# Kernel tuning notes

Measured on AMD Instinct MI355X. Metric: run time of the kernel, lower is better.

Reference implementation:

```python
import jax, jax.numpy as jnp
import numpy as np

N_NODES = 100000
N_EDGES = 3200000


def gcn_conv(x, src, dst, W, b, n):
    # x: [N, Fin] -> linear transform then symmetric-normalized scatter-add (PyG GCNConv)
    xw = x @ W  # [N, Fout]
    loop = jnp.arange(n, dtype=src.dtype)
    s = jnp.concatenate([src, loop])  # add self-loops
    d = jnp.concatenate([dst, loop])
    deg = jax.ops.segment_sum(jnp.ones_like(s, dtype=xw.dtype), d, num_segments=n)
    dinv = jnp.where(deg > 0, jax.lax.rsqrt(deg), 0.0)
    norm = dinv[s] * dinv[d]  # [E+N]
    out = jax.ops.segment_sum(xw[s] * norm[:, None], d, num_segments=n)
    return out + b


def setup_inputs() -> dict:
    key = jax.random.key(0)
    ks = jax.random.split(key, 11)
    x = jax.random.normal(ks[0], (N_NODES, 2), dtype=jnp.float32)
    edge_index = jax.random.randint(ks[1], (2, N_EDGES), 0, N_NODES, dtype=jnp.int64)
    W1 = jax.random.normal(ks[2], (2, 32), dtype=jnp.float32) * 0.5
    b1 = jax.random.normal(ks[3], (32,), dtype=jnp.float32) * 0.1
    W2 = jax.random.normal(ks[4], (32, 32), dtype=jnp.float32) * 0.18
    b2 = jax.random.normal(ks[5], (32,), dtype=jnp.float32) * 0.1
    Wf1 = jax.random.normal(ks[6], (32, 32), dtype=jnp.float32) * 0.18
    bf1 = jax.random.normal(ks[7], (32,), dtype=jnp.float32) * 0.1
    Wf2 = jax.random.normal(ks[8], (32, 1), dtype=jnp.float32) * 0.18
    bf2 = jax.random.normal(ks[9], (1,), dtype=jnp.float32) * 0.1
    return {"x": x, "edge_index": edge_index, "W1": W1, "b1": b1, "W2": W2,
            "b2": b2, "Wf1": Wf1, "bf1": bf1, "Wf2": Wf2, "bf2": bf2}


def reference(x, edge_index, W1, b1, W2, b2, Wf1, bf1, Wf2, bf2):
    n = x.shape[0]
    src, dst = edge_index[0], edge_index[1]
    h = jax.nn.relu(gcn_conv(x, src, dst, W1, b1, n))
    h = jax.nn.relu(gcn_conv(h, src, dst, W2, b2, n))
    h = jax.nn.relu(h @ Wf1 + bf1)
    return h @ Wf2 + bf2  # [N, 1]
```

## Files before the change

kernel.cpp:

```cpp
#include <hip/hip_runtime.h>

#define NGRP 512
#define CAP  6656
#define EPB  8192
#define SRC_BITS 17
#define SRC_MASK 0x1FFFF

static __device__ __forceinline__ unsigned short f2bf(float f) {
    unsigned u = __float_as_uint(f);
    return (unsigned short)((u + 0x7FFFu + ((u >> 16) & 1u)) >> 16);
}
static __device__ __forceinline__ float bf2f_lo(unsigned u) { return __uint_as_float(u << 16); }
static __device__ __forceinline__ float bf2f_hi(unsigned u) { return __uint_as_float(u & 0xFFFF0000u); }


__global__ void k_init(int* gcursor) {
    int t = threadIdx.x;
    gcursor[t] = t * CAP;
}

__global__ __launch_bounds__(512) void k_partition(const int* __restrict__ ei, int* gcursor,
                                                   unsigned* __restrict__ pairs,
                                                   int E, int n, int GN) {
    __shared__ int cnt[NGRP];
    __shared__ int cur[NGRP];
    int tid = threadIdx.x;
    cnt[tid] = 0;
    __syncthreads();
    int base = blockIdx.x * EPB;
    for (int k = tid; k < EPB; k += 512) {
        int e = base + k;
        if (e < E) {
            int s = ei[e], d = ei[E + e];
            if ((unsigned)s < (unsigned)n && (unsigned)d < (unsigned)n)
                atomicAdd(&cnt[d / GN], 1);
        }
    }
    __syncthreads();
    { int c = cnt[tid]; cur[tid] = c ? atomicAdd(&gcursor[tid], c) : 0; }
    __syncthreads();
    for (int k = tid; k < EPB; k += 512) {
        int e = base + k;
        if (e < E) {
            int s = ei[e], d = ei[E + e];
            if ((unsigned)s < (unsigned)n && (unsigned)d < (unsigned)n) {
                int g = d / GN;
                int w = atomicAdd(&cur[g], 1);
                if (w < (g + 1) * CAP)
                    pairs[w] = ((unsigned)(d - g * GN) << SRC_BITS) | (unsigned)s;
            }
        }
    }
}

__global__ __launch_bounds__(512) void k_build(const int* __restrict__ gcursor,
                                               const unsigned* __restrict__ pairs,
                                               const float2* __restrict__ x2,
                                               int* __restrict__ rowStart, int* __restrict__ rowEnd,
                                               int* __restrict__ srclist, float* __restrict__ dinv,
                                               float2* __restrict__ z, int n, int GN) {
    __shared__ unsigned pl[CAP];
    __shared__ int cnt[512];
    __shared__ int cur[512];
    int g = blockIdx.x;
    int t = threadIdx.x;
    int gbeg = g * CAP;
    int gend = gcursor[g];
    int cape = gbeg + CAP;
    if (gend > cape) gend = cape;
    int m = gend - gbeg;
    cnt[t] = 0;
    __syncthreads();
    for (int k = t; k < m; k += 512) {
        unsigned v = pairs[gbeg + k];
        pl[k] = v;
        atomicAdd(&cnt[(v >> SRC_BITS) & 511], 1);
    }
    __syncthreads();
    int c = cnt[t];
    for (int off = 1; off < 512; off <<= 1) {
        int add = (t >= off) ? cnt[t - off] : 0;
        __syncthreads();
        cnt[t] += add;
        __syncthreads();
    }
    int excl = cnt[t] - c;
    int node = g * GN + t;
    if (t < GN && node < n) {
        int st = gbeg + excl;
        rowStart[node] = st;
        rowEnd[node] = st + c;
        float di = rsqrtf(1.0f + (float)c);
        dinv[node] = di;
        float2 xv = x2[node];
        z[node] = make_float2(xv.x * di, xv.y * di);
    }
    cur[t] = excl;
    __syncthreads();
    for (int k = t; k < m; k += 512) {
        unsigned v = pl[k];
        int dl = (v >> SRC_BITS) & 511;
        int pos = atomicAdd(&cur[dl], 1);
        srclist[gbeg + pos] = (int)(v & SRC_MASK);
    }
}


__global__ void k_gather2f(const int* __restrict__ rowStart, const int* __restrict__ rowEnd,
                           const int* __restrict__ srclist, const float2* __restrict__ z,
                           float2* __restrict__ agg, int n) {
    int w = blockIdx.x * (blockDim.x >> 6) + (threadIdx.x >> 6);
    if (w >= n) return;
    int lane = threadIdx.x & 63;
    int start = rowStart[w], end = rowEnd[w];
    float ax = 0.f, ay = 0.f;
    for (int e = start + lane; e < end; e += 64) {
        int s = srclist[e];
        float2 v = z[s];
        ax += v.x; ay += v.y;
    }
#pragma unroll
    for (int m = 1; m < 64; m <<= 1) {
        ax += __shfl_xor(ax, m, 64);
        ay += __shfl_xor(ay, m, 64);
    }
    if (lane == 0) {
        float2 v = z[w];
        agg[w] = make_float2(ax + v.x, ay + v.y);
    }
}

__global__ void k_mid1(const float2* __restrict__ agg, const float* __restrict__ dinv,
                       const float* __restrict__ W1, const float* __restrict__ b1,
                       const float* __restrict__ W2, unsigned short* __restrict__ y_bf, int n) {
    __shared__ float sW[1024];
    __shared__ float sh[8][33];
    int tid = threadIdx.x;
    for (int k = tid; k < 1024; k += 256) sW[k] = W2[k];
    int ln = tid >> 5, f = tid & 31;
    int i = blockIdx.x * 8 + ln;
    float h = 0.f, di = 0.f;
    if (i < n) {
        di = dinv[i];
        float2 a = agg[i];
        h = di * (a.x * W1[f] + a.y * W1[32 + f]) + b1[f];
        h = h > 0.f ? h : 0.f;
    }
    sh[ln][f] = h;
    __syncthreads();
    if (i < n) {
        float acc = 0.f;
#pragma unroll
        for (int k = 0; k < 32; ++k) acc += sh[ln][k] * sW[k * 32 + f];
        y_bf[(size_t)i * 32 + f] = f2bf(acc * di);
    }
}

__global__ void k_gather(const int* __restrict__ rowStart, const int* __restrict__ rowEnd,
                         const int* __restrict__ srclist, const uint4* __restrict__ y4,
                         float4* __restrict__ acc4, int n) {
    int w = blockIdx.x * (blockDim.x >> 6) + (threadIdx.x >> 6);
    if (w >= n) return;
    int lane = threadIdx.x & 63;
    int slot = lane >> 2, q = lane & 3;
    int start = rowStart[w], end = rowEnd[w];
    float a0 = 0.f, a1 = 0.f, a2 = 0.f, a3 = 0.f, a4 = 0.f, a5 = 0.f, a6 = 0.f, a7 = 0.f;
    for (int e = start + slot; e < end; e += 16) {
        int s = srclist[e];
        uint4 v = y4[(size_t)s * 4 + q];
        a0 += bf2f_lo(v.x); a1 += bf2f_hi(v.x);
        a2 += bf2f_lo(v.y); a3 += bf2f_hi(v.y);
        a4 += bf2f_lo(v.z); a5 += bf2f_hi(v.z);
        a6 += bf2f_lo(v.w); a7 += bf2f_hi(v.w);
    }
#pragma unroll
    for (int m = 4; m < 64; m <<= 1) {
        a0 += __shfl_xor(a0, m, 64);
        a1 += __shfl_xor(a1, m, 64);
        a2 += __shfl_xor(a2, m, 64);
        a3 += __shfl_xor(a3, m, 64);
        a4 += __shfl_xor(a4, m, 64);
        a5 += __shfl_xor(a5, m, 64);
        a6 += __shfl_xor(a6, m, 64);
        a7 += __shfl_xor(a7, m, 64);
    }
    if (slot == 0) {
        uint4 v = y4[(size_t)w * 4 + q];
        a0 += bf2f_lo(v.x); a1 += bf2f_hi(v.x);
        a2 += bf2f_lo(v.y); a3 += bf2f_hi(v.y);
        a4 += bf2f_lo(v.z); a5 += bf2f_hi(v.z);
        a6 += bf2f_lo(v.w); a7 += bf2f_hi(v.w);
        size_t base = (size_t)w * 8 + q * 2;
        acc4[base]     = make_float4(a0, a1, a2, a3);
        acc4[base + 1] = make_float4(a4, a5, a6, a7);
    }
}

__global__ void k_final(const float* __restrict__ acc, const float* __restrict__ dinv,
                        const float* __restrict__ b2, const float* __restrict__ Wf1,
                        const float* __restrict__ bf1, const float* __restrict__ Wf2,
                        const float* __restrict__ bf2, float* __restrict__ out, int n) {
    __shared__ float sW[1024];
    __shared__ float sh[8][33];
    int tid = threadIdx.x;
    for (int k = tid; k < 1024; k += 256) sW[k] = Wf1[k];
    int ln = tid >> 5, f = tid & 31;
    int i = blockIdx.x * 8 + ln;
    float h = 0.f;
    if (i < n) {
        h = dinv[i] * acc[(size_t)i * 32 + f] + b2[f];
        h = h > 0.f ? h : 0.f;
    }
    sh[ln][f] = h;
    __syncthreads();
    float p = 0.f;
    if (i < n) {
        float a = bf1[f];
#pragma unroll
        for (int k = 0; k < 32; ++k) a += sh[ln][k] * sW[k * 32 + f];
        a = a > 0.f ? a : 0.f;
        p = a * Wf2[f];
    }
#pragma unroll
    for (int m = 16; m >= 1; m >>= 1) p += __shfl_xor(p, m, 64);
    if (f == 0 && i < n) out[i] = p + bf2[0];
}


extern "C" void kernel_launch(void* const* d_in, const int* in_sizes, int n_in,
                              void* d_out, int out_size, void* d_ws, size_t ws_size,
                              hipStream_t stream) {
    const float* x   = (const float*)d_in[0];
    const int*   ei  = (const int*)d_in[1];
    const float* W1  = (const float*)d_in[2];
    const float* b1  = (const float*)d_in[3];
    const float* W2  = (const float*)d_in[4];
    const float* b2  = (const float*)d_in[5];
    const float* Wf1 = (const float*)d_in[6];
    const float* bf1 = (const float*)d_in[7];
    const float* Wf2 = (const float*)d_in[8];
    const float* bf2 = (const float*)d_in[9];
    float* out = (float*)d_out;

    int n = in_sizes[0] / 2;
    int E = in_sizes[1] / 2;
    int GN = (n + NGRP - 1) / NGRP;

    float* wsf = (float*)d_ws;
    int*    srclist  = (int*)wsf;
    size_t  o = (size_t)NGRP * CAP;
    int*    rowStart = (int*)(wsf + o);     o += n;
    int*    rowEnd   = (int*)(wsf + o);     o += n;
    float*  dinv     = wsf + o;             o += n;
    float2* z        = (float2*)(wsf + o);  o += 2 * (size_t)n;
    float2* agg      = (float2*)(wsf + o);  o += 2 * (size_t)n;
    int*    gcursor  = (int*)(wsf + o);     o += NGRP;
    o = (o + 3) & ~(size_t)3;
    float*  acc      = wsf + o;             o += 32 * (size_t)n;
    unsigned short* y_bf = (unsigned short*)(wsf + o);
    unsigned* pairs = (unsigned*)acc;

    const int B = 256;
    int nblk = (E + EPB - 1) / EPB;

    k_init<<<1, NGRP, 0, stream>>>(gcursor);
    k_partition<<<nblk, 512, 0, stream>>>(ei, gcursor, pairs, E, n, GN);
    k_build<<<NGRP, 512, 0, stream>>>(gcursor, pairs, (const float2*)x, rowStart, rowEnd,
                                      srclist, dinv, z, n, GN);

    k_gather2f<<<(n + 3) / 4, B, 0, stream>>>(rowStart, rowEnd, srclist, z, agg, n);
    k_mid1<<<(n + 7) / 8, B, 0, stream>>>(agg, dinv, W1, b1, W2, y_bf, n);

    k_gather<<<(n + 3) / 4, B, 0, stream>>>(rowStart, rowEnd, srclist, (const uint4*)y_bf,
                                            (float4*)acc, n);

    k_final<<<(n + 7) / 8, B, 0, stream>>>(acc, dinv, b2, Wf1, bf1, Wf2, bf2, out, n);
}
```

Before: 178.6 us.

## Split bf16 features into two halves gathered separately; cache edges in registers

The second-layer feature table is split into two 16-feature bf16 planes, and the neighbor gather runs as two passes, each touching a 3.2MB table instead of 6.4MB. The intent is to keep each pass's random-access working set resident in cache. The cost is reading the CSR source list twice plus an extra launch. The partition kernel also keeps each thread's 16 edges in registers, so the second pass no longer reloads the edge index from global memory.

```diff
diff --git a/kernel.cpp b/kernel.cpp
--- a/kernel.cpp
+++ b/kernel.cpp
@@ -3,6 +3,7 @@
 #define NGRP 512
 #define CAP  6656
 #define EPB  8192
+#define NE   16
 #define SRC_BITS 17
 #define SRC_MASK 0x1FFFF
 
@@ -15,8 +16,7 @@
 
 
 __global__ void k_init(int* gcursor) {
-    int t = threadIdx.x;
-    gcursor[t] = t * CAP;
+    gcursor[threadIdx.x] = threadIdx.x * CAP;
 }
 
 __global__ __launch_bounds__(512) void k_partition(const int* __restrict__ ei, int* gcursor,
@@ -28,27 +28,31 @@
     cnt[tid] = 0;
     __syncthreads();
     int base = blockIdx.x * EPB;
-    for (int k = tid; k < EPB; k += 512) {
-        int e = base + k;
+    int sreg[NE], dreg[NE];
+#pragma unroll
+    for (int k = 0; k < NE; ++k) {
+        int e = base + tid + k * 512;
+        int d = -1, s = 0;
         if (e < E) {
-            int s = ei[e], d = ei[E + e];
+            s = ei[e];
+            d = ei[E + e];
             if ((unsigned)s < (unsigned)n && (unsigned)d < (unsigned)n)
                 atomicAdd(&cnt[d / GN], 1);
+            else d = -1;
         }
+        sreg[k] = s; dreg[k] = d;
     }
     __syncthreads();
     { int c = cnt[tid]; cur[tid] = c ? atomicAdd(&gcursor[tid], c) : 0; }
     __syncthreads();
-    for (int k = tid; k < EPB; k += 512) {
-        int e = base + k;
-        if (e < E) {
-            int s = ei[e], d = ei[E + e];
-            if ((unsigned)s < (unsigned)n && (unsigned)d < (unsigned)n) {
-                int g = d / GN;
-                int w = atomicAdd(&cur[g], 1);
-                if (w < (g + 1) * CAP)
-                    pairs[w] = ((unsigned)(d - g * GN) << SRC_BITS) | (unsigned)s;
-            }
+#pragma unroll
+    for (int k = 0; k < NE; ++k) {
+        int d = dreg[k];
+        if (d >= 0) {
+            int g = d / GN;
+            int w = atomicAdd(&cur[g], 1);
+            if (w < (g + 1) * CAP)
+                pairs[w] = ((unsigned)(d - g * GN) << SRC_BITS) | (unsigned)sreg[k];
         }
     }
 }
@@ -132,7 +136,8 @@
 
 __global__ void k_mid1(const float2* __restrict__ agg, const float* __restrict__ dinv,
                        const float* __restrict__ W1, const float* __restrict__ b1,
-                       const float* __restrict__ W2, unsigned short* __restrict__ y_bf, int n) {
+                       const float* __restrict__ W2, unsigned short* __restrict__ y0,
+                       unsigned short* __restrict__ y1, int n) {
     __shared__ float sW[1024];
     __shared__ float sh[8][33];
     int tid = threadIdx.x;
@@ -152,29 +157,30 @@
         float acc = 0.f;
 #pragma unroll
         for (int k = 0; k < 32; ++k) acc += sh[ln][k] * sW[k * 32 + f];
-        y_bf[(size_t)i * 32 + f] = f2bf(acc * di);
-    }
-}
-
-__global__ void k_gather(const int* __restrict__ rowStart, const int* __restrict__ rowEnd,
-                         const int* __restrict__ srclist, const uint4* __restrict__ y4,
-                         float4* __restrict__ acc4, int n) {
+        unsigned short* yp = (f < 16) ? y0 : y1;
+        yp[(size_t)i * 16 + (f & 15)] = f2bf(acc * di);
+    }
+}
+
+__global__ void k_gather_half(const int* __restrict__ rowStart, const int* __restrict__ rowEnd,
+                              const int* __restrict__ srclist, const uint4* __restrict__ yh,
+                              float4* __restrict__ acc4, int n, int p) {
     int w = blockIdx.x * (blockDim.x >> 6) + (threadIdx.x >> 6);
     if (w >= n) return;
     int lane = threadIdx.x & 63;
-    int slot = lane >> 2, q = lane & 3;
+    int slot = lane >> 1, q = lane & 1;
     int start = rowStart[w], end = rowEnd[w];
     float a0 = 0.f, a1 = 0.f, a2 = 0.f, a3 = 0.f, a4 = 0.f, a5 = 0.f, a6 = 0.f, a7 = 0.f;
-    for (int e = start + slot; e < end; e += 16) {
+    for (int e = start + slot; e < end; e += 32) {
         int s = srclist[e];
-        uint4 v = y4[(size_t)s * 4 + q];
+        uint4 v = yh[(size_t)s * 2 + q];
         a0 += bf2f_lo(v.x); a1 += bf2f_hi(v.x);
         a2 += bf2f_lo(v.y); a3 += bf2f_hi(v.y);
         a4 += bf2f_lo(v.z); a5 += bf2f_hi(v.z);
         a6 += bf2f_lo(v.w); a7 += bf2f_hi(v.w);
     }
 #pragma unroll
-    for (int m = 4; m < 64; m <<= 1) {
+    for (int m = 2; m < 64; m <<= 1) {
         a0 += __shfl_xor(a0, m, 64);
         a1 += __shfl_xor(a1, m, 64);
         a2 += __shfl_xor(a2, m, 64);
@@ -185,14 +191,14 @@
         a7 += __shfl_xor(a7, m, 64);
     }
     if (slot == 0) {
-        uint4 v = y4[(size_t)w * 4 + q];
+        uint4 v = yh[(size_t)w * 2 + q];
         a0 += bf2f_lo(v.x); a1 += bf2f_hi(v.x);
         a2 += bf2f_lo(v.y); a3 += bf2f_hi(v.y);
         a4 += bf2f_lo(v.z); a5 += bf2f_hi(v.z);
         a6 += bf2f_lo(v.w); a7 += bf2f_hi(v.w);
-        size_t base = (size_t)w * 8 + q * 2;
-        acc4[base]     = make_float4(a0, a1, a2, a3);
-        acc4[base + 1] = make_float4(a4, a5, a6, a7);
+        float4* dst = acc4 + (size_t)w * 8 + p * 4 + q * 2;
+        dst[0] = make_float4(a0, a1, a2, a3);
+        dst[1] = make_float4(a4, a5, a6, a7);
     }
 }
 
@@ -257,7 +263,8 @@
     int*    gcursor  = (int*)(wsf + o);     o += NGRP;
     o = (o + 3) & ~(size_t)3;
     float*  acc      = wsf + o;             o += 32 * (size_t)n;
-    unsigned short* y_bf = (unsigned short*)(wsf + o);
+    unsigned short* y0 = (unsigned short*)(wsf + o);
+    unsigned short* y1 = y0 + (size_t)n * 16;
     unsigned* pairs = (unsigned*)acc;
 
     const int B = 256;
@@ -269,10 +276,12 @@
                                       srclist, dinv, z, n, GN);
 
     k_gather2f<<<(n + 3) / 4, B, 0, stream>>>(rowStart, rowEnd, srclist, z, agg, n);
-    k_mid1<<<(n + 7) / 8, B, 0, stream>>>(agg, dinv, W1, b1, W2, y_bf, n);
-
-    k_gather<<<(n + 3) / 4, B, 0, stream>>>(rowStart, rowEnd, srclist, (const uint4*)y_bf,
-                                            (float4*)acc, n);
+    k_mid1<<<(n + 7) / 8, B, 0, stream>>>(agg, dinv, W1, b1, W2, y0, y1, n);
+
+    k_gather_half<<<(n + 3) / 4, B, 0, stream>>>(rowStart, rowEnd, srclist, (const uint4*)y0,
+                                                 (float4*)acc, n, 0);
+    k_gather_half<<<(n + 3) / 4, B, 0, stream>>>(rowStart, rowEnd, srclist, (const uint4*)y1,
+                                                 (float4*)acc, n, 1);
 
     k_final<<<(n + 7) / 8, B, 0, stream>>>(acc, dinv, b2, Wf1, bf1, Wf2, bf2, out, n);
 }
```

After: 211.5 us. 1.18x slower.
